# Optimization experiments

Measured on AMD Instinct MI355X. Metric: run time of the kernel, lower is better.

Reference implementation:

```python
import jax, jax.numpy as jnp
import numpy as np
from jax import lax

B, T, K = 512, 1024, 48


def setup_inputs() -> dict:
    key = jax.random.key(0)
    k1, k2, k3, k4, k5, k6 = jax.random.split(key, 6)
    emissions = jax.random.normal(k1, (B, T, K), dtype=jnp.float32)
    lengths = jax.random.randint(k2, (B,), 1, T + 1)  # every seq has >=1 valid step
    raw_tags = jax.random.randint(k3, (B, T), 0, K)
    pos = jnp.arange(T)[None, :]
    tags = jnp.where(pos < lengths[:, None], raw_tags, -1)  # -1 = pad, as in pad_sequence
    u = lambda k, s: jax.random.uniform(k, s, minval=-0.1, maxval=0.1, dtype=jnp.float32)
    return {
        "emissions": emissions,
        "tags": tags,
        "start_transitions": u(k4, (K,)),
        "end_transitions": u(k5, (K,)),
        "transitions": u(k6, (K, K)),
    }


def _crf_loss(emissions, tags, mask, start_transitions, end_transitions, transitions):
    """-sum_b log p(tags_b | emissions_b)  (torchcrf reduction='sum')."""
    maskf = mask.astype(emissions.dtype)
    safe_tags = jnp.where(mask, tags, 0)
    b_idx = jnp.arange(emissions.shape[0])

    # ---- numerator: score of the gold path ----
    emit_scores = jnp.take_along_axis(emissions, safe_tags[:, :, None], axis=2)[..., 0]  # [B,T]
    trans_scores = transitions[safe_tags[:, :-1], safe_tags[:, 1:]]  # [B,T-1]
    score = start_transitions[safe_tags[:, 0]] + emit_scores[:, 0]
    score = score + jnp.sum((trans_scores + emit_scores[:, 1:]) * maskf[:, 1:], axis=1)
    lengths = mask.sum(axis=1)
    last_tags = safe_tags[b_idx, lengths - 1]
    score = score + end_transitions[last_tags]

    # ---- denominator: log partition via forward algorithm (scan over time) ----
    em_t = jnp.transpose(emissions, (1, 0, 2))  # [T,B,K]
    mk_t = jnp.transpose(mask, (1, 0))          # [T,B]

    def step(alpha, xm):
        e, m = xm  # e:[B,K], m:[B]
        nxt = jax.nn.logsumexp(alpha[:, :, None] + transitions[None], axis=1) + e
        return jnp.where(m[:, None], nxt, alpha), None

    alpha0 = start_transitions[None, :] + em_t[0]
    alpha, _ = lax.scan(step, alpha0, (em_t[1:], mk_t[1:]))
    log_z = jax.nn.logsumexp(alpha + end_transitions[None, :], axis=1)
    return -jnp.sum(score - log_z)


def _viterbi(emissions, mask, start_transitions, end_transitions, transitions):
    em_t = jnp.transpose(emissions, (1, 0, 2))  # [T,B,K]
    mk_t = jnp.transpose(mask, (1, 0))          # [T,B]
    ident = jnp.arange(K, dtype=jnp.int32)[None, :]  # identity backpointer for padded steps

    def vstep(alpha, xm):
        e, m = xm
        scores = alpha[:, :, None] + transitions[None]  # [B,K(prev),K(cur)]
        best_prev = jnp.argmax(scores, axis=1).astype(jnp.int32)  # [B,K]
        nxt = jnp.max(scores, axis=1) + e
        alpha2 = jnp.where(m[:, None], nxt, alpha)
        bp = jnp.where(m[:, None], best_prev, ident)
        return alpha2, bp

    alpha0 = start_transitions[None, :] + em_t[0]
    alpha, bps = lax.scan(vstep, alpha0, (em_t[1:], mk_t[1:]))  # bps: [T-1,B,K]
    best_last = jnp.argmax(alpha + end_transitions[None, :], axis=1).astype(jnp.int32)  # [B]

    def btstep(cur, bp):
        prev = jnp.take_along_axis(bp, cur[:, None], axis=1)[:, 0]
        return prev, cur

    first_tag, rest = lax.scan(btstep, best_last, bps, reverse=True)  # rest[t] = tag at t+1
    best_tags = jnp.concatenate([first_tag[None], rest], axis=0).T  # [B,T]
    return jnp.where(mask, best_tags, -1)


def reference(emissions, tags, start_transitions, end_transitions, transitions):
    mask = tags > -1
    loss = _crf_loss(emissions, tags, mask, start_transitions, end_transitions, transitions)
    pred_tags = _viterbi(emissions, mask, start_transitions, end_transitions, transitions)
    return loss, pred_tags
```

## Files before the change

kernel.cpp:

```cpp
#include <hip/hip_runtime.h>

#define BB 512
#define TT 1024
#define KK 48
#define NINF (-1e30f)

__device__ __forceinline__ float rfirst(float v) {
    return __int_as_float(__builtin_amdgcn_readfirstlane(__float_as_int(v)));
}

__global__ __launch_bounds__(128, 1) void crf_main(
    const float* __restrict__ em,
    const int*   __restrict__ tags,
    const float* __restrict__ st,
    const float* __restrict__ en,
    const float* __restrict__ tr,
    float* __restrict__ out,
    float* __restrict__ ws)
{
    __shared__ unsigned char s_bp[TT * KK];
    __shared__ unsigned char s_path[TT];
    __shared__ float s_avb[2][64];

    const int b    = blockIdx.x;
    const int tid  = threadIdx.x;
    const int lane = tid & 63;
    const int wid  = tid >> 6;

    const float* emb = em + (size_t)b * TT * KK;
    const int*   tgb = tags + (size_t)b * TT;

    int cnt = 0;
    for (int t = lane; t < TT; t += 64) cnt += (tgb[t] > -1) ? 1 : 0;
#pragma unroll
    for (int off = 32; off >= 1; off >>= 1) cnt += __shfl_xor(cnt, off);
    const int len = cnt;

    const bool act = lane < KK;
    const int  jj  = act ? lane : (KK - 1);

    const int S = len - 1;

    if (wid == 0) {
        float sc = 0.f;
        for (int t = lane; t < len; t += 64) {
            int tg = tgb[t];
            sc += emb[t * KK + tg];
            if (t > 0) sc += tr[tgb[t - 1] * KK + tg];
        }
#pragma unroll
        for (int off = 32; off >= 1; off >>= 1) sc += __shfl_xor(sc, off);
        const float score = sc + st[tgb[0]] + en[tgb[len - 1]];

        float eTc[KK];
#pragma unroll
        for (int i = 0; i < KK; ++i) eTc[i] = __expf(tr[i * KK + jj]);

        float a0 = st[jj] + emb[jj];
        float C  = rfirst(a0);
        float p  = __expf(a0 - C);

        const float4* S4 = (const float4*)(&s_avb[0][0]);

        float e[2];
        {
            int t1 = (1 < len) ? 1 : (len - 1);
            int t2 = (2 < len) ? 2 : (len - 1);
            e[1] = emb[(size_t)t1 * KK + jj];
            e[0] = emb[(size_t)t2 * KK + jj];
        }

#define FSTEP(t_, RENORM) {                                                  \
        const float eS = e[(t_) & 1];                                        \
        s_avb[0][lane] = p;              \
        float z0 = 0.f, z1 = 0.f, z2 = 0.f, z3 = 0.f;                        \
        float z4 = 0.f, z5 = 0.f, z6 = 0.f, z7 = 0.f;                        \
        _Pragma("unroll")                                                    \
        for (int q = 0; q < 6; ++q) {                                        \
            float4 v0 = S4[2 * q], v1 = S4[2 * q + 1];                       \
            z0 = fmaf(v0.x, eTc[8 * q + 0], z0);                             \
            z1 = fmaf(v0.y, eTc[8 * q + 1], z1);                             \
            z2 = fmaf(v0.z, eTc[8 * q + 2], z2);                             \
            z3 = fmaf(v0.w, eTc[8 * q + 3], z3);                             \
            z4 = fmaf(v1.x, eTc[8 * q + 4], z4);                             \
            z5 = fmaf(v1.y, eTc[8 * q + 5], z5);                             \
            z6 = fmaf(v1.z, eTc[8 * q + 6], z6);                             \
            z7 = fmaf(v1.w, eTc[8 * q + 7], z7);                             \
        }                                                                    \
        p = (((z0 + z1) + (z2 + z3)) + ((z4 + z5) + (z6 + z7)))              \
            * __expf(eS);                                                    \
        if (RENORM) {                                                        \
            float m = rfirst(p);                                             \
            p *= __frcp_rn(m);                                               \
            C += __logf(m);                                                  \
        }                                                                    \
        int tn = (t_) + 2; tn = (tn < len) ? tn : (len - 1);                 \
        e[(t_) & 1] = emb[(size_t)tn * KK + jj];                             \
    }

        {
            int t = 1;
            for (; t + 4 <= S + 1; t += 4) {
                FSTEP(t, 0) FSTEP(t + 1, 0) FSTEP(t + 2, 0) FSTEP(t + 3, 1)
            }
            for (; t <= S; ++t) FSTEP(t, 1)
        }
#undef FSTEP

        float y = act ? (p * __expf(en[jj])) : 0.f;
#pragma unroll
        for (int off = 32; off >= 1; off >>= 1) y += __shfl_xor(y, off);
        float logz = C + __logf(y);
        if (lane == 0) ws[b] = score - logz;
    } else {
        float Tc[KK];
#pragma unroll
        for (int i = 0; i < KK; ++i) Tc[i] = tr[i * KK + jj];

        float av = st[jj] + emb[jj];

        const float4* S4 = (const float4*)(&s_avb[1][0]);

        float e[2];
        {
            int t1 = (1 < len) ? 1 : (len - 1);
            int t2 = (2 < len) ? 2 : (len - 1);
            e[1] = emb[(size_t)t1 * KK + jj];
            e[0] = emb[(size_t)t2 * KK + jj];
        }

        float xA[KK], xB[KK];
        float MA = 0.f, MB = 0.f;

#define MAXPHASE(X, MV, t_) {                                                \
        const float eS = e[(t_) & 1];                                        \
        s_avb[1][lane] = av;             \
        _Pragma("unroll")                                                    \
        for (int q = 0; q < 12; ++q) {                                       \
            float4 v = S4[q];                                                \
            X[4 * q + 0] = v.x + Tc[4 * q + 0];                              \
            X[4 * q + 1] = v.y + Tc[4 * q + 1];                              \
            X[4 * q + 2] = v.z + Tc[4 * q + 2];                              \
            X[4 * q + 3] = v.w + Tc[4 * q + 3];                              \
        }                                                                    \
        float l1[16];                                                        \
        _Pragma("unroll")                                                    \
        for (int q = 0; q < 16; ++q)                                         \
            l1[q] = fmaxf(fmaxf(X[3 * q], X[3 * q + 1]), X[3 * q + 2]);      \
        float l2[6];                                                         \
        _Pragma("unroll")                                                    \
        for (int q = 0; q < 5; ++q)                                          \
            l2[q] = fmaxf(fmaxf(l1[3 * q], l1[3 * q + 1]), l1[3 * q + 2]);   \
        l2[5] = l1[15];                                                      \
        MV = fmaxf(fmaxf(fmaxf(l2[0], l2[1]), l2[2]),                        \
                   fmaxf(fmaxf(l2[3], l2[4]), l2[5]));                       \
        av = MV + eS;                                                        \
        int tn = (t_) + 2; tn = (tn < len) ? tn : (len - 1);                 \
        e[(t_) & 1] = emb[(size_t)tn * KK + jj];                             \
    }

#define ARGPHASE(X, MV, t_) {                                                \
        unsigned u[KK];                                                      \
        _Pragma("unroll")                                                    \
        for (int i = 0; i < KK; ++i)                                         \
            u[i] = (unsigned)__float_as_int(X[i] - MV) | (unsigned)i;        \
        unsigned m1[16];                                                     \
        _Pragma("unroll")                                                    \
        for (int q = 0; q < 16; ++q)                                         \
            m1[q] = min(min(u[3 * q], u[3 * q + 1]), u[3 * q + 2]);          \
        unsigned m2[6];                                                      \
        _Pragma("unroll")                                                    \
        for (int q = 0; q < 5; ++q)                                          \
            m2[q] = min(min(m1[3 * q], m1[3 * q + 1]), m1[3 * q + 2]);       \
        m2[5] = m1[15];                                                      \
        unsigned bi = min(min(min(m2[0], m2[1]), m2[2]),                     \
                          min(min(m2[3], m2[4]), m2[5]));                    \
        s_bp[(t_) * KK + jj] = (unsigned char)bi;    \
    }

        if (S >= 1) {
            int t = 1;
            MAXPHASE(xA, MA, 1)
            while (t + 2 <= S) {
                MAXPHASE(xB, MB, t + 1)
                ARGPHASE(xA, MA, t)
                MAXPHASE(xA, MA, t + 2)
                ARGPHASE(xB, MB, t + 1)
                t += 2;
            }
            if (t + 1 <= S) {
                MAXPHASE(xB, MB, t + 1)
                ARGPHASE(xA, MA, t)
                ARGPHASE(xB, MB, t + 1)
            } else {
                ARGPHASE(xA, MA, t)
            }
        }
#undef MAXPHASE
#undef ARGPHASE

        float v = act ? (av + en[jj]) : NINF;
        float M = v;
#pragma unroll
        for (int off = 32; off >= 1; off >>= 1) M = fmaxf(M, __shfl_xor(M, off));
        unsigned long long msk = __ballot(v == M);
        int cur = __ffsll(msk) - 1;
        s_path[len - 1] = (unsigned char)cur;

        int t = len - 1;
        while (t >= 1) {
            const int n = (t < 8) ? t : 8;
            unsigned r[8];
#pragma unroll
            for (int k = 0; k < 8; ++k)
                r[k] = (k < n) ? (unsigned)s_bp[(t - k) * KK + jj] : 0u;
#pragma unroll
            for (int k = 0; k < 8; ++k) {
                if (k < n) {
                    cur = __builtin_amdgcn_readlane((int)r[k], cur);
                    if (lane == 0) s_path[t - k - 1] = (unsigned char)cur;
                }
            }
            t -= n;
        }

        float* ob = out + 1 + (size_t)b * TT;
        for (int tt = lane; tt < TT; tt += 64)
            ob[tt] = (tt < len) ? (float)s_path[tt] : -1.0f;
    }
}

__global__ __launch_bounds__(512) void loss_reduce(const float* __restrict__ ws,
                                                   float* __restrict__ out)
{
    __shared__ float sh[8];
    const int lane = threadIdx.x & 63;
    const int w    = threadIdx.x >> 6;
    float s = ws[threadIdx.x];
#pragma unroll
    for (int off = 32; off >= 1; off >>= 1) s += __shfl_xor(s, off);
    if (lane == 0) sh[w] = s;
    __syncthreads();
    if (threadIdx.x == 0) {
        float tot = 0.f;
        for (int i = 0; i < 8; ++i) tot += sh[i];
        out[0] = -tot;
    }
}

extern "C" void kernel_launch(void* const* d_in, const int* in_sizes, int n_in,
                              void* d_out, int out_size, void* d_ws, size_t ws_size,
                              hipStream_t stream)
{
    const float* em   = (const float*)d_in[0];
    const int*   tags = (const int*)d_in[1];
    const float* st   = (const float*)d_in[2];
    const float* en   = (const float*)d_in[3];
    const float* tr   = (const float*)d_in[4];
    float* out = (float*)d_out;
    float* wsf = (float*)d_ws;

    hipLaunchKernelGGL(crf_main, dim3(BB), dim3(128), 0, stream,
                       em, tags, st, en, tr, out, wsf);
    hipLaunchKernelGGL(loss_reduce, dim3(1), dim3(512), 0, stream, wsf, out);
}
```

Before: 509.1 us.

## Pack four sequences per block and spill Viterbi backpointers to global workspace

After: 667.2 us. 31.1% more time.

```diff
diff --git a/kernel.cpp b/kernel.cpp
--- a/kernel.cpp
+++ b/kernel.cpp
@@ -9,13 +9,242 @@
     return __int_as_float(__builtin_amdgcn_readfirstlane(__float_as_int(v)));
 }
 
+#define FSTEP_BODY(S4, RENORM, ES)                                           \
+    {                                                                        \
+        float z0 = 0.f, z1 = 0.f, z2 = 0.f, z3 = 0.f;                        \
+        float z4 = 0.f, z5 = 0.f, z6 = 0.f, z7 = 0.f;                        \
+        _Pragma("unroll")                                                    \
+        for (int q_ = 0; q_ < 6; ++q_) {                                     \
+            float4 v0 = S4[2 * q_], v1 = S4[2 * q_ + 1];                     \
+            z0 = fmaf(v0.x, eTc[8 * q_ + 0], z0);                            \
+            z1 = fmaf(v0.y, eTc[8 * q_ + 1], z1);                            \
+            z2 = fmaf(v0.z, eTc[8 * q_ + 2], z2);                            \
+            z3 = fmaf(v0.w, eTc[8 * q_ + 3], z3);                            \
+            z4 = fmaf(v1.x, eTc[8 * q_ + 4], z4);                            \
+            z5 = fmaf(v1.y, eTc[8 * q_ + 5], z5);                            \
+            z6 = fmaf(v1.z, eTc[8 * q_ + 6], z6);                            \
+            z7 = fmaf(v1.w, eTc[8 * q_ + 7], z7);                            \
+        }                                                                    \
+        p = (((z0 + z1) + (z2 + z3)) + ((z4 + z5) + (z6 + z7)))              \
+            * __expf(ES);                                                    \
+        if (RENORM) {                                                        \
+            float m_ = rfirst(p);                                            \
+            p *= __frcp_rn(m_);                                              \
+            C += __logf(m_);                                                 \
+        }                                                                    \
+    }
+
+#define MAXPHASE_BODY(SB, S4, X, MV, ES)                                     \
+    {                                                                        \
+        SB[lane] = av;                   \
+        _Pragma("unroll")                                                    \
+        for (int q_ = 0; q_ < 12; ++q_) {                                    \
+            float4 v_ = S4[q_];                                              \
+            X[4 * q_ + 0] = v_.x + Tc[4 * q_ + 0];                           \
+            X[4 * q_ + 1] = v_.y + Tc[4 * q_ + 1];                           \
+            X[4 * q_ + 2] = v_.z + Tc[4 * q_ + 2];                           \
+            X[4 * q_ + 3] = v_.w + Tc[4 * q_ + 3];                           \
+        }                                                                    \
+        float l1[16];                                                        \
+        _Pragma("unroll")                                                    \
+        for (int q_ = 0; q_ < 16; ++q_)                                      \
+            l1[q_] = fmaxf(fmaxf(X[3 * q_], X[3 * q_ + 1]), X[3 * q_ + 2]);  \
+        float l2[6];                                                         \
+        _Pragma("unroll")                                                    \
+        for (int q_ = 0; q_ < 5; ++q_)                                       \
+            l2[q_] = fmaxf(fmaxf(l1[3 * q_], l1[3 * q_ + 1]),                \
+                           l1[3 * q_ + 2]);                                  \
+        l2[5] = l1[15];                                                      \
+        MV = fmaxf(fmaxf(fmaxf(l2[0], l2[1]), l2[2]),                        \
+                   fmaxf(fmaxf(l2[3], l2[4]), l2[5]));                       \
+        av = MV + (ES);                                                      \
+    }
+
+#define ARGPHASE_BODY(X, MV, STORE_STMT)                                     \
+    {                                                                        \
+        unsigned u[KK];                                                      \
+        _Pragma("unroll")                                                    \
+        for (int i_ = 0; i_ < KK; ++i_)                                      \
+            u[i_] = (unsigned)__float_as_int(X[i_] - MV) | (unsigned)i_;     \
+        unsigned m1[16];                                                     \
+        _Pragma("unroll")                                                    \
+        for (int q_ = 0; q_ < 16; ++q_)                                      \
+            m1[q_] = min(min(u[3 * q_], u[3 * q_ + 1]), u[3 * q_ + 2]);      \
+        unsigned m2[6];                                                      \
+        _Pragma("unroll")                                                    \
+        for (int q_ = 0; q_ < 5; ++q_)                                       \
+            m2[q_] = min(min(m1[3 * q_], m1[3 * q_ + 1]), m1[3 * q_ + 2]);   \
+        m2[5] = m1[15];                                                      \
+        unsigned bi = min(min(min(m2[0], m2[1]), m2[2]),                     \
+                          min(min(m2[3], m2[4]), m2[5]));                    \
+        STORE_STMT;                                                          \
+    }
+
+__global__ __launch_bounds__(512, 1) void crf_fast(
+    const float* __restrict__ em, const int* __restrict__ tags,
+    const float* __restrict__ st, const float* __restrict__ en,
+    const float* __restrict__ tr, float* __restrict__ out,
+    float* __restrict__ wsl, unsigned char* __restrict__ gbp)
+{
+    __shared__ unsigned char s_path[4][TT];
+    __shared__ float s_avb[8][64];
+
+    const int tid  = threadIdx.x;
+    const int lane = tid & 63;
+    const int wid  = tid >> 6;
+    const int q    = wid >> 1;
+    const int role = wid & 1;
+    const int b    = blockIdx.x * 4 + q;
+
+    const float* emb = em + (size_t)b * TT * KK;
+    const int*   tgb = tags + (size_t)b * TT;
+
+    int cnt = 0;
+    for (int t = lane; t < TT; t += 64) cnt += (tgb[t] > -1) ? 1 : 0;
+#pragma unroll
+    for (int off = 32; off >= 1; off >>= 1) cnt += __shfl_xor(cnt, off);
+    const int len = cnt;
+
+    const bool act = lane < KK;
+    const int  jj  = act ? lane : (KK - 1);
+    const int  S   = len - 1;
+
+    float* sb = &s_avb[wid][0];
+    const float4* S4 = (const float4*)sb;
+
+    if (role == 0) {
+        float sc = 0.f;
+        for (int t = lane; t < len; t += 64) {
+            int tg = tgb[t];
+            sc += emb[t * KK + tg];
+            if (t > 0) sc += tr[tgb[t - 1] * KK + tg];
+        }
+#pragma unroll
+        for (int off = 32; off >= 1; off >>= 1) sc += __shfl_xor(sc, off);
+        const float score = sc + st[tgb[0]] + en[tgb[len - 1]];
+
+        float eTc[KK];
+#pragma unroll
+        for (int i = 0; i < KK; ++i) eTc[i] = __expf(tr[i * KK + jj]);
+
+        float a0 = st[jj] + emb[jj];
+        float C  = rfirst(a0);
+        float p  = __expf(a0 - C);
+
+        float e[2];
+        {
+            int t1 = (1 < len) ? 1 : (len - 1);
+            int t2 = (2 < len) ? 2 : (len - 1);
+            e[1] = emb[(size_t)t1 * KK + jj];
+            e[0] = emb[(size_t)t2 * KK + jj];
+        }
+
+#define FSTEP(t_, RENORM) {                                                  \
+        const float eS = e[(t_) & 1];                                        \
+        sb[lane] = p;                                                        \
+        FSTEP_BODY(S4, RENORM, eS)                                           \
+        int tn = (t_) + 2; tn = (tn < len) ? tn : (len - 1);                 \
+        e[(t_) & 1] = emb[(size_t)tn * KK + jj];                             \
+    }
+        {
+            int t = 1;
+            for (; t + 4 <= S + 1; t += 4) {
+                FSTEP(t, 0) FSTEP(t + 1, 0) FSTEP(t + 2, 0) FSTEP(t + 3, 1)
+            }
+            for (; t <= S; ++t) FSTEP(t, 1)
+        }
+#undef FSTEP
+
+        float y = act ? (p * __expf(en[jj])) : 0.f;
+#pragma unroll
+        for (int off = 32; off >= 1; off >>= 1) y += __shfl_xor(y, off);
+        float logz = C + __logf(y);
+        if (lane == 0) wsl[b] = score - logz;
+    } else {
+        float Tc[KK];
+#pragma unroll
+        for (int i = 0; i < KK; ++i) Tc[i] = tr[i * KK + jj];
+
+        float av = st[jj] + emb[jj];
+
+        float e[2];
+        {
+            int t1 = (1 < len) ? 1 : (len - 1);
+            int t2 = (2 < len) ? 2 : (len - 1);
+            e[1] = emb[(size_t)t1 * KK + jj];
+            e[0] = emb[(size_t)t2 * KK + jj];
+        }
+
+        float xA[KK], xB[KK];
+        float MA = 0.f, MB = 0.f;
+        unsigned char* bpb = gbp + (size_t)b * TT * KK;
+
+#define MAXPHASE(X, MV, t_) {                                                \
+        const float eS = e[(t_) & 1];                                        \
+        MAXPHASE_BODY(sb, S4, X, MV, eS)                                     \
+        int tn = (t_) + 2; tn = (tn < len) ? tn : (len - 1);                 \
+        e[(t_) & 1] = emb[(size_t)tn * KK + jj];                             \
+    }
+#define ARGPHASE(X, MV, t_) \
+        ARGPHASE_BODY(X, MV, bpb[(size_t)(t_) * KK + jj] = (unsigned char)bi)
+
+        if (S >= 1) {
+            int t = 1;
+            MAXPHASE(xA, MA, 1)
+            while (t + 2 <= S) {
+                MAXPHASE(xB, MB, t + 1)
+                ARGPHASE(xA, MA, t)
+                MAXPHASE(xA, MA, t + 2)
+                ARGPHASE(xB, MB, t + 1)
+                t += 2;
+            }
+            if (t + 1 <= S) {
+                MAXPHASE(xB, MB, t + 1)
+                ARGPHASE(xA, MA, t)
+                ARGPHASE(xB, MB, t + 1)
+            } else {
+                ARGPHASE(xA, MA, t)
+            }
+        }
+#undef MAXPHASE
+#undef ARGPHASE
+
+        float v = act ? (av + en[jj]) : NINF;
+        float M = v;
+#pragma unroll
+        for (int off = 32; off >= 1; off >>= 1) M = fmaxf(M, __shfl_xor(M, off));
+        unsigned long long msk = __ballot(v == M);
+        int cur = __ffsll(msk) - 1;
+        s_path[q][len - 1] = (unsigned char)cur;
+
+        asm volatile("s_waitcnt vmcnt(0)" ::: "memory");
+        int t = len - 1;
+        while (t >= 1) {
+            const int n = (t < 8) ? t : 8;
+            unsigned r[8];
+#pragma unroll
+            for (int k = 0; k < 8; ++k)
+                r[k] = (k < n) ? (unsigned)bpb[(size_t)(t - k) * KK + jj] : 0u;
+#pragma unroll
+            for (int k = 0; k < 8; ++k) {
+                if (k < n) {
+                    cur = __builtin_amdgcn_readlane((int)r[k], cur);
+                    if (lane == 0) s_path[q][t - k - 1] = (unsigned char)cur;
+                }
+            }
+            t -= n;
+        }
+
+        float* ob = out + 1 + (size_t)b * TT;
+        for (int tt = lane; tt < TT; tt += 64)
+            ob[tt] = (tt < len) ? (float)s_path[q][tt] : -1.0f;
+    }
+}
+
 __global__ __launch_bounds__(128, 1) void crf_main(
-    const float* __restrict__ em,
-    const int*   __restrict__ tags,
-    const float* __restrict__ st,
-    const float* __restrict__ en,
-    const float* __restrict__ tr,
-    float* __restrict__ out,
+    const float* __restrict__ em, const int* __restrict__ tags,
+    const float* __restrict__ st, const float* __restrict__ en,
+    const float* __restrict__ tr, float* __restrict__ out,
     float* __restrict__ ws)
 {
     __shared__ unsigned char s_bp[TT * KK];
@@ -38,8 +267,7 @@
 
     const bool act = lane < KK;
     const int  jj  = act ? lane : (KK - 1);
-
-    const int S = len - 1;
+    const int  S   = len - 1;
 
     if (wid == 0) {
         float sc = 0.f;
@@ -60,7 +288,8 @@
         float C  = rfirst(a0);
         float p  = __expf(a0 - C);
 
-        const float4* S4 = (const float4*)(&s_avb[0][0]);
+        float* sb = &s_avb[0][0];
+        const float4* S4 = (const float4*)sb;
 
         float e[2];
         {
@@ -72,32 +301,11 @@
 
 #define FSTEP(t_, RENORM) {                                                  \
         const float eS = e[(t_) & 1];                                        \
-        s_avb[0][lane] = p;              \
-        float z0 = 0.f, z1 = 0.f, z2 = 0.f, z3 = 0.f;                        \
-        float z4 = 0.f, z5 = 0.f, z6 = 0.f, z7 = 0.f;                        \
-        _Pragma("unroll")                                                    \
-        for (int q = 0; q < 6; ++q) {                                        \
-            float4 v0 = S4[2 * q], v1 = S4[2 * q + 1];                       \
-            z0 = fmaf(v0.x, eTc[8 * q + 0], z0);                             \
-            z1 = fmaf(v0.y, eTc[8 * q + 1], z1);                             \
-            z2 = fmaf(v0.z, eTc[8 * q + 2], z2);                             \
-            z3 = fmaf(v0.w, eTc[8 * q + 3], z3);                             \
-            z4 = fmaf(v1.x, eTc[8 * q + 4], z4);                             \
-            z5 = fmaf(v1.y, eTc[8 * q + 5], z5);                             \
-            z6 = fmaf(v1.z, eTc[8 * q + 6], z6);                             \
-            z7 = fmaf(v1.w, eTc[8 * q + 7], z7);                             \
-        }                                                                    \
-        p = (((z0 + z1) + (z2 + z3)) + ((z4 + z5) + (z6 + z7)))              \
-            * __expf(eS);                                                    \
-        if (RENORM) {                                                        \
-            float m = rfirst(p);                                             \
-            p *= __frcp_rn(m);                                               \
-            C += __logf(m);                                                  \
-        }                                                                    \
+        sb[lane] = p;                                                        \
+        FSTEP_BODY(S4, RENORM, eS)                                           \
         int tn = (t_) + 2; tn = (tn < len) ? tn : (len - 1);                 \
         e[(t_) & 1] = emb[(size_t)tn * KK + jj];                             \
     }
-
         {
             int t = 1;
             for (; t + 4 <= S + 1; t += 4) {
@@ -119,7 +327,8 @@
 
         float av = st[jj] + emb[jj];
 
-        const float4* S4 = (const float4*)(&s_avb[1][0]);
+        float* sb = &s_avb[1][0];
+        const float4* S4 = (const float4*)sb;
 
         float e[2];
         {
@@ -134,49 +343,12 @@
 
 #define MAXPHASE(X, MV, t_) {                                                \
         const float eS = e[(t_) & 1];                                        \
-        s_avb[1][lane] = av;             \
-        _Pragma("unroll")                                                    \
-        for (int q = 0; q < 12; ++q) {                                       \
-            float4 v = S4[q];                                                \
-            X[4 * q + 0] = v.x + Tc[4 * q + 0];                              \
-            X[4 * q + 1] = v.y + Tc[4 * q + 1];                              \
-            X[4 * q + 2] = v.z + Tc[4 * q + 2];                              \
-            X[4 * q + 3] = v.w + Tc[4 * q + 3];                              \
-        }                                                                    \
-        float l1[16];                                                        \
-        _Pragma("unroll")                                                    \
-        for (int q = 0; q < 16; ++q)                                         \
-            l1[q] = fmaxf(fmaxf(X[3 * q], X[3 * q + 1]), X[3 * q + 2]);      \
-        float l2[6];                                                         \
-        _Pragma("unroll")                                                    \
-        for (int q = 0; q < 5; ++q)                                          \
-            l2[q] = fmaxf(fmaxf(l1[3 * q], l1[3 * q + 1]), l1[3 * q + 2]);   \
-        l2[5] = l1[15];                                                      \
-        MV = fmaxf(fmaxf(fmaxf(l2[0], l2[1]), l2[2]),                        \
-                   fmaxf(fmaxf(l2[3], l2[4]), l2[5]));                       \
-        av = MV + eS;                                                        \
+        MAXPHASE_BODY(sb, S4, X, MV, eS)                                     \
         int tn = (t_) + 2; tn = (tn < len) ? tn : (len - 1);                 \
         e[(t_) & 1] = emb[(size_t)tn * KK + jj];                             \
     }
-
-#define ARGPHASE(X, MV, t_) {                                                \
-        unsigned u[KK];                                                      \
-        _Pragma("unroll")                                                    \
-        for (int i = 0; i < KK; ++i)                                         \
-            u[i] = (unsigned)__float_as_int(X[i] - MV) | (unsigned)i;        \
-        unsigned m1[16];                                                     \
-        _Pragma("unroll")                                                    \
-        for (int q = 0; q < 16; ++q)                                         \
-            m1[q] = min(min(u[3 * q], u[3 * q + 1]), u[3 * q + 2]);          \
-        unsigned m2[6];                                                      \
-        _Pragma("unroll")                                                    \
-        for (int q = 0; q < 5; ++q)                                          \
-            m2[q] = min(min(m1[3 * q], m1[3 * q + 1]), m1[3 * q + 2]);       \
-        m2[5] = m1[15];                                                      \
-        unsigned bi = min(min(min(m2[0], m2[1]), m2[2]),                     \
-                          min(min(m2[3], m2[4]), m2[5]));                    \
-        s_bp[(t_) * KK + jj] = (unsigned char)bi;    \
-    }
+#define ARGPHASE(X, MV, t_) \
+        ARGPHASE_BODY(X, MV, s_bp[(size_t)(t_) * KK + jj] = (unsigned char)bi)
 
         if (S >= 1) {
             int t = 1;
@@ -213,7 +385,7 @@
             unsigned r[8];
 #pragma unroll
             for (int k = 0; k < 8; ++k)
-                r[k] = (k < n) ? (unsigned)s_bp[(t - k) * KK + jj] : 0u;
+                r[k] = (k < n) ? (unsigned)s_bp[(size_t)(t - k) * KK + jj] : 0u;
 #pragma unroll
             for (int k = 0; k < 8; ++k) {
                 if (k < n) {
@@ -258,9 +430,18 @@
     const float* en   = (const float*)d_in[3];
     const float* tr   = (const float*)d_in[4];
     float* out = (float*)d_out;
-    float* wsf = (float*)d_ws;
-
-    hipLaunchKernelGGL(crf_main, dim3(BB), dim3(128), 0, stream,
-                       em, tags, st, en, tr, out, wsf);
-    hipLaunchKernelGGL(loss_reduce, dim3(1), dim3(512), 0, stream, wsf, out);
+
+    const size_t BPBYTES = (size_t)BB * TT * KK;
+    if (ws_size >= BPBYTES + BB * sizeof(float)) {
+        unsigned char* gbp = (unsigned char*)d_ws;
+        float* wsl = (float*)((char*)d_ws + BPBYTES);
+        hipLaunchKernelGGL(crf_fast, dim3(BB / 4), dim3(512), 0, stream,
+                           em, tags, st, en, tr, out, wsl, gbp);
+        hipLaunchKernelGGL(loss_reduce, dim3(1), dim3(512), 0, stream, wsl, out);
+    } else {
+        float* wsf = (float*)d_ws;
+        hipLaunchKernelGGL(crf_main, dim3(BB), dim3(128), 0, stream,
+                           em, tags, st, en, tr, out, wsf);
+        hipLaunchKernelGGL(loss_reduce, dim3(1), dim3(512), 0, stream, wsf, out);
+    }
 }
```
